# Optimization experiments

Measured on AMD Instinct MI355X. Metric: run time of the kernel, lower is better.

## Reference

```python
import jax, jax.numpy as jnp
import numpy as np

OUT_FEATURES = 4096
IN_FEATURES = 4096
GROUP_SIZE = 32
NUM_GROUPS = (OUT_FEATURES * IN_FEATURES) // GROUP_SIZE  # 524288, divisible by 8
PACKED_PER_GROUP = GROUP_SIZE * 3 // 8  # 12


def dequantize_3bit(x_packed, maxvals):
    # x_packed: [NUM_GROUPS * 12] int, values in [0,256) (uint8 bit patterns)
    # maxvals:  [NUM_GROUPS] float32 group scales
    G = NUM_GROUPS
    # view as [G, 4, 3]: 4 byte-triplets per group, each encoding 8 3-bit values
    p = x_packed.reshape(G, GROUP_SIZE // 8, 3)
    b0, b1, b2 = p[..., 0], p[..., 1], p[..., 2]
    v0 = b0 & 7
    v1 = (b0 >> 3) & 7
    v2 = ((b0 >> 6) & 3) | ((b1 & 1) << 2)
    v3 = (b1 >> 1) & 7
    v4 = (b1 >> 4) & 7
    v5 = ((b1 >> 7) & 1) | ((b2 & 3) << 1)
    v6 = (b2 >> 2) & 7
    v7 = (b2 >> 5) & 7
    q = jnp.stack([v0, v1, v2, v3, v4, v5, v6, v7], axis=-1)  # [G, 4, 8]
    q = q.reshape(G, GROUP_SIZE).astype(jnp.float32)
    x_norm = (q / 7.0 * 2.0 - 1.0) * maxvals[:, None]
    return x_norm.reshape(-1)  # [G * GROUP_SIZE]


def setup_inputs() -> dict:
    key = jax.random.key(0)
    k1, k2, k3, k4 = jax.random.split(key, 4)
    x = jax.random.normal(k1, (2, 2048, IN_FEATURES), dtype=jnp.float32)
    weight_q3 = jax.random.randint(k2, (NUM_GROUPS * PACKED_PER_GROUP,), 0, 256, dtype=jnp.int32)
    weight_norm = jax.random.uniform(k3, (NUM_GROUPS,), dtype=jnp.float32)
    bias = jax.random.normal(k4, (OUT_FEATURES,), dtype=jnp.float32)
    return {"x": x, "weight_q3": weight_q3, "weight_norm": weight_norm, "bias": bias}


def reference(x, weight_q3, weight_norm, bias):
    w_flat = dequantize_3bit(weight_q3, weight_norm)
    weight = w_flat[: OUT_FEATURES * IN_FEATURES].reshape(OUT_FEATURES, IN_FEATURES)
    # F.linear: y = x @ W.T + b
    return jnp.einsum("bsi,oi->bso", x, weight) + bias
```

## Files before the change

### kernel.cpp

```cpp
#include <hip/hip_runtime.h>

typedef unsigned short u16;
typedef unsigned int u32;

typedef __bf16 bf16x8 __attribute__((ext_vector_type(8)));
typedef float f32x4 __attribute__((ext_vector_type(4)));

#define OUT_F 4096
#define IN_F 4096
#define M_ROWS 4096
#define NUM_GROUPS ((OUT_F * IN_F) / 32)


__device__ __forceinline__ u16 f2bf(float f) {
    union { float f; u32 u; } c; c.f = f;
    u32 u = c.u;
    u += 0x7fffu + ((u >> 16) & 1u);
    return (u16)(u >> 16);
}

__device__ __forceinline__ u32 pk2(float a, float b) {
    return (u32)f2bf(a) | ((u32)f2bf(b) << 16);
}

__device__ __forceinline__ void async_copy16(const u16* g, u16* l) {
    __builtin_amdgcn_global_load_lds(
        (const __attribute__((address_space(1))) u32*)g,
        (__attribute__((address_space(3))) u32*)l,
        16, 0, 0);
}

__device__ __forceinline__ u32 lds_addr(const u16* p) {
    return (u32)(uintptr_t)(const __attribute__((address_space(3))) u16*)p;
}

__global__ __launch_bounds__(256) void prep_kernel(
        const float* __restrict__ x, const int* __restrict__ q,
        const float* __restrict__ scales,
        u16* __restrict__ W, u16* __restrict__ Xb) {
    int bid = blockIdx.x;
    int tid = threadIdx.x;
    if (bid < 8192) {
        int t = bid * 256 + tid;
        int b0 = q[3 * t];
        int b1 = q[3 * t + 1];
        int b2 = q[3 * t + 2];
        float mv = scales[t >> 2];
        float s = mv * (2.0f / 7.0f);
        float o = -mv;

        int v0 = b0 & 7;
        int v1 = (b0 >> 3) & 7;
        int v2 = ((b0 >> 6) & 3) | ((b1 & 1) << 2);
        int v3 = (b1 >> 1) & 7;
        int v4 = (b1 >> 4) & 7;
        int v5 = ((b1 >> 7) & 1) | ((b2 & 3) << 1);
        int v6 = (b2 >> 2) & 7;
        int v7 = (b2 >> 5) & 7;
        uint4 w;
        w.x = pk2(fmaf((float)v0, s, o), fmaf((float)v1, s, o));
        w.y = pk2(fmaf((float)v2, s, o), fmaf((float)v3, s, o));
        w.z = pk2(fmaf((float)v4, s, o), fmaf((float)v5, s, o));
        w.w = pk2(fmaf((float)v6, s, o), fmaf((float)v7, s, o));
        ((uint4*)W)[t] = w;
    } else {
        int i = (bid - 8192) * 256 + tid;
        const float4* p = (const float4*)x + (size_t)i * 2;
        float4 u = p[0], v = p[1];
        uint4 w;
        w.x = pk2(u.x, u.y);
        w.y = pk2(u.z, u.w);
        w.z = pk2(v.x, v.y);
        w.w = pk2(v.z, v.w);
        ((uint4*)Xb)[i] = w;
    }
}

__global__ __launch_bounds__(256, 2) void gemm_bt_kernel(
        const u16* __restrict__ A, const u16* __restrict__ B,
        const float* __restrict__ bias, float* __restrict__ C) {
    __shared__ u16 sA[256 * 64];
    __shared__ u16 sB[128 * 64];

    const int tid = threadIdx.x;
    const int lane = tid & 63;
    const int w = tid >> 6;
    const int wr = w >> 1;
    const int wc = w & 1;
    const int ln = lane & 15;
    const int quad = lane >> 4;
    const int lnx = ln & 7;

    const int lin = blockIdx.x;
    const int wg = (lin & 7) * 64 + (lin >> 3);
    const int mb = (wg >> 5) * 256;
    const int nb = (wg & 31) * 128;

    int offg[8], offl[8];
#pragma unroll
    for (int p = 0; p < 8; ++p) {
        int s = p * 256 + tid;
        int rl = s >> 3, pc = s & 7;
        int lc = pc ^ (rl & 7);
        offg[p] = rl * IN_F + lc * 8;
        offl[p] = s * 8;
    }
    const u16* baseA = A + (size_t)mb * IN_F;
    const u16* baseB = B + (size_t)nb * IN_F;

    const u32 sAb = lds_addr(sA);
    const u32 sBb = lds_addr(sB);
    const u32 aB0 = sAb + (u32)((wr * 128 + ln) * 128 + ((quad ^ lnx) * 16));
    const u32 aB1 = sAb + (u32)((wr * 128 + ln) * 128 + (((4 + quad) ^ lnx) * 16));
    const u32 bB0 = sBb + (u32)((wc * 64 + ln) * 128 + ((quad ^ lnx) * 16));
    const u32 bB1 = sBb + (u32)((wc * 64 + ln) * 128 + (((4 + quad) ^ lnx) * 16));

    float bj[4];
#pragma unroll
    for (int j = 0; j < 4; ++j)
        bj[j] = bias[nb + wc * 64 + j * 16 + ln];

    f32x4 acc[8][4];
#pragma unroll
    for (int i = 0; i < 8; ++i)
#pragma unroll
        for (int j = 0; j < 4; ++j) acc[i][j] = (f32x4)0.0f;

    bf16x8 av[4][2];
    bf16x8 bv[4][2];

#define DSR(dst, base, IMM) \
    asm volatile("ds_read_b128 %0, %1 offset:" #IMM \
                 : "=v"(dst) : "v"(base))

#define WAITG(N) \
    asm volatile("s_waitcnt lgkmcnt(" #N ")"); \
    __builtin_amdgcn_sched_barrier(0);

#define MROW(IR, ACR) \
    acc[ACR][0] = __builtin_amdgcn_mfma_f32_16x16x32_bf16( \
        av[IR][0], bv[0][0], acc[ACR][0], 0, 0, 0); \
    acc[ACR][1] = __builtin_amdgcn_mfma_f32_16x16x32_bf16( \
        av[IR][0], bv[1][0], acc[ACR][1], 0, 0, 0); \
    acc[ACR][2] = __builtin_amdgcn_mfma_f32_16x16x32_bf16( \
        av[IR][0], bv[2][0], acc[ACR][2], 0, 0, 0); \
    acc[ACR][3] = __builtin_amdgcn_mfma_f32_16x16x32_bf16( \
        av[IR][0], bv[3][0], acc[ACR][3], 0, 0, 0); \
    acc[ACR][0] = __builtin_amdgcn_mfma_f32_16x16x32_bf16( \
        av[IR][1], bv[0][1], acc[ACR][0], 0, 0, 0); \
    acc[ACR][1] = __builtin_amdgcn_mfma_f32_16x16x32_bf16( \
        av[IR][1], bv[1][1], acc[ACR][1], 0, 0, 0); \
    acc[ACR][2] = __builtin_amdgcn_mfma_f32_16x16x32_bf16( \
        av[IR][1], bv[2][1], acc[ACR][2], 0, 0, 0); \
    acc[ACR][3] = __builtin_amdgcn_mfma_f32_16x16x32_bf16( \
        av[IR][1], bv[3][1], acc[ACR][3], 0, 0, 0);

#pragma unroll
    for (int p = 0; p < 8; ++p)
        async_copy16(baseA + offg[p], &sA[offl[p]]);
#pragma unroll
    for (int p = 0; p < 4; ++p)
        async_copy16(baseB + offg[p], &sB[offl[p]]);
    asm volatile("s_waitcnt vmcnt(0)");
    __builtin_amdgcn_s_barrier();

#pragma unroll 1
    for (int t = 0; t < 64; ++t) {
        DSR(bv[0][0], bB0, 0);     DSR(bv[0][1], bB1, 0);
        DSR(bv[1][0], bB0, 2048);  DSR(bv[1][1], bB1, 2048);
        DSR(bv[2][0], bB0, 4096);  DSR(bv[2][1], bB1, 4096);
        DSR(bv[3][0], bB0, 6144);  DSR(bv[3][1], bB1, 6144);
        DSR(av[0][0], aB0, 0);     DSR(av[0][1], aB1, 0);
        DSR(av[1][0], aB0, 2048);  DSR(av[1][1], aB1, 2048);
        DSR(av[2][0], aB0, 4096);  DSR(av[2][1], aB1, 4096);
        DSR(av[3][0], aB0, 6144);  DSR(av[3][1], aB1, 6144);
        __builtin_amdgcn_s_setprio(1);
        WAITG(6); MROW(0, 0);
        WAITG(4); MROW(1, 1);
        WAITG(2); MROW(2, 2);
        WAITG(0); MROW(3, 3);
        __builtin_amdgcn_s_setprio(0);

        DSR(av[0][0], aB0, 8192);   DSR(av[0][1], aB1, 8192);
        DSR(av[1][0], aB0, 10240);  DSR(av[1][1], aB1, 10240);
        DSR(av[2][0], aB0, 12288);  DSR(av[2][1], aB1, 12288);
        DSR(av[3][0], aB0, 14336);  DSR(av[3][1], aB1, 14336);
        __builtin_amdgcn_s_setprio(1);
        WAITG(6); MROW(0, 4);
        WAITG(4); MROW(1, 5);
        WAITG(2); MROW(2, 6);
        WAITG(0); MROW(3, 7);
        __builtin_amdgcn_s_setprio(0);

        __builtin_amdgcn_s_barrier();
        if (t < 63) {
            const int ko1 = (t + 1) << 6;
#pragma unroll
            for (int p = 0; p < 8; ++p)
                async_copy16(baseA + offg[p] + ko1, &sA[offl[p]]);
#pragma unroll
            for (int p = 0; p < 4; ++p)
                async_copy16(baseB + offg[p] + ko1, &sB[offl[p]]);
        }
        asm volatile("s_waitcnt vmcnt(0)");
        __builtin_amdgcn_s_barrier();
    }

#undef DSR
#undef WAITG
#undef MROW

#pragma unroll
    for (int i = 0; i < 8; ++i) {
        const int mrow = mb + wr * 128 + i * 16 + quad * 4;
#pragma unroll
        for (int j = 0; j < 4; ++j) {
            const int col = nb + wc * 64 + j * 16 + ln;
            float* cp = C + (size_t)mrow * OUT_F + col;
#pragma unroll
            for (int r = 0; r < 4; ++r)
                cp[(size_t)r * OUT_F] = acc[i][j][r] + bj[j];
        }
    }
}

extern "C" void kernel_launch(void* const* d_in, const int* in_sizes, int n_in,
                              void* d_out, int out_size, void* d_ws, size_t ws_size,
                              hipStream_t stream) {
    const float* x = (const float*)d_in[0];
    const int* wq = (const int*)d_in[1];
    const float* wn = (const float*)d_in[2];
    const float* bias = (const float*)d_in[3];
    float* out = (float*)d_out;

    u16* Wb = (u16*)d_ws;
    u16* Xb = Wb + (size_t)OUT_F * IN_F;

    prep_kernel<<<16384, 256, 0, stream>>>(x, wq, wn, Wb, Xb);
    gemm_bt_kernel<<<512, 256, 0, stream>>>(Xb, Wb, bias, out);
}
```

Baseline: 141.0 us.

## Load B operand directly from global to registers and double-buffer A tile in LDS

The weight (B) operand is no longer staged through shared memory. Each lane now issues global_load_dwordx4 straight into its MFMA operand registers, and the next K-step's B loads are issued before the barrier. The A tile becomes double-buffered in LDS so the next tile's async copy overlaps the current compute, dropping one barrier and the full vmcnt(0) drain per iteration. This cuts LDS traffic and synchronisation, but adds uncoalesced-ish strided global reads for B, hand-managed vmcnt counting, and one redundant wrap-around prefetch on the final iteration.

Result: slower. 195.5 us (+38.6%).

```diff
diff --git a/kernel.cpp b/kernel.cpp
--- a/kernel.cpp
+++ b/kernel.cpp
@@ -2,6 +2,7 @@
 
 typedef unsigned short u16;
 typedef unsigned int u32;
+typedef unsigned long long u64;
 
 typedef __bf16 bf16x8 __attribute__((ext_vector_type(8)));
 typedef float f32x4 __attribute__((ext_vector_type(4)));
@@ -10,6 +11,8 @@
 #define IN_F 4096
 #define M_ROWS 4096
 #define NUM_GROUPS ((OUT_F * IN_F) / 32)
+
+#define TILE_A_E (256 * 64)
 
 
 __device__ __forceinline__ u16 f2bf(float f) {
@@ -79,8 +82,7 @@
 __global__ __launch_bounds__(256, 2) void gemm_bt_kernel(
         const u16* __restrict__ A, const u16* __restrict__ B,
         const float* __restrict__ bias, float* __restrict__ C) {
-    __shared__ u16 sA[256 * 64];
-    __shared__ u16 sB[128 * 64];
+    __shared__ u16 sA[2 * TILE_A_E];
 
     const int tid = threadIdx.x;
     const int lane = tid & 63;
@@ -106,14 +108,16 @@
         offl[p] = s * 8;
     }
     const u16* baseA = A + (size_t)mb * IN_F;
-    const u16* baseB = B + (size_t)nb * IN_F;
 
     const u32 sAb = lds_addr(sA);
-    const u32 sBb = lds_addr(sB);
     const u32 aB0 = sAb + (u32)((wr * 128 + ln) * 128 + ((quad ^ lnx) * 16));
     const u32 aB1 = sAb + (u32)((wr * 128 + ln) * 128 + (((4 + quad) ^ lnx) * 16));
-    const u32 bB0 = sBb + (u32)((wc * 64 + ln) * 128 + ((quad ^ lnx) * 16));
-    const u32 bB1 = sBb + (u32)((wc * 64 + ln) * 128 + (((4 + quad) ^ lnx) * 16));
+
+    u64 bAddr[4];
+#pragma unroll
+    for (int j = 0; j < 4; ++j)
+        bAddr[j] = (u64)(const char*)(B + (size_t)(nb + wc * 64 + j * 16 + ln) * IN_F)
+                 + (u64)(quad * 16);
 
     float bj[4];
 #pragma unroll
@@ -133,9 +137,38 @@
     asm volatile("ds_read_b128 %0, %1 offset:" #IMM \
                  : "=v"(dst) : "v"(base))
 
-#define WAITG(N) \
-    asm volatile("s_waitcnt lgkmcnt(" #N ")"); \
-    __builtin_amdgcn_sched_barrier(0);
+#define GLB0(dst, ap) \
+    asm volatile("global_load_dwordx4 %0, %1, off" : "=v"(dst) : "v"(ap))
+#define GLB1(dst, ap) \
+    asm volatile("global_load_dwordx4 %0, %1, off offset:64" : "=v"(dst) : "v"(ap))
+
+#define WVL(V, L) \
+    asm volatile("s_waitcnt vmcnt(" #V ") lgkmcnt(" #L ")"); \
+    __builtin_amdgcn_sched_barrier(0);
+#define WV(V) \
+    asm volatile("s_waitcnt vmcnt(" #V ")"); \
+    __builtin_amdgcn_sched_barrier(0);
+#define WL(L) \
+    asm volatile("s_waitcnt lgkmcnt(" #L ")"); \
+    __builtin_amdgcn_sched_barrier(0);
+
+#define MCOL(J) \
+    acc[0][J] = __builtin_amdgcn_mfma_f32_16x16x32_bf16( \
+        av[0][0], bv[J][0], acc[0][J], 0, 0, 0); \
+    acc[1][J] = __builtin_amdgcn_mfma_f32_16x16x32_bf16( \
+        av[1][0], bv[J][0], acc[1][J], 0, 0, 0); \
+    acc[2][J] = __builtin_amdgcn_mfma_f32_16x16x32_bf16( \
+        av[2][0], bv[J][0], acc[2][J], 0, 0, 0); \
+    acc[3][J] = __builtin_amdgcn_mfma_f32_16x16x32_bf16( \
+        av[3][0], bv[J][0], acc[3][J], 0, 0, 0); \
+    acc[0][J] = __builtin_amdgcn_mfma_f32_16x16x32_bf16( \
+        av[0][1], bv[J][1], acc[0][J], 0, 0, 0); \
+    acc[1][J] = __builtin_amdgcn_mfma_f32_16x16x32_bf16( \
+        av[1][1], bv[J][1], acc[1][J], 0, 0, 0); \
+    acc[2][J] = __builtin_amdgcn_mfma_f32_16x16x32_bf16( \
+        av[2][1], bv[J][1], acc[2][J], 0, 0, 0); \
+    acc[3][J] = __builtin_amdgcn_mfma_f32_16x16x32_bf16( \
+        av[3][1], bv[J][1], acc[3][J], 0, 0, 0);
 
 #define MROW(IR, ACR) \
     acc[ACR][0] = __builtin_amdgcn_mfma_f32_16x16x32_bf16( \
@@ -155,60 +188,78 @@
     acc[ACR][3] = __builtin_amdgcn_mfma_f32_16x16x32_bf16( \
         av[IR][1], bv[3][1], acc[ACR][3], 0, 0, 0);
 
+#define ISSUE_B() \
+    GLB0(bv[0][0], bAddr[0]); GLB1(bv[0][1], bAddr[0]); \
+    GLB0(bv[1][0], bAddr[1]); GLB1(bv[1][1], bAddr[1]); \
+    GLB0(bv[2][0], bAddr[2]); GLB1(bv[2][1], bAddr[2]); \
+    GLB0(bv[3][0], bAddr[3]); GLB1(bv[3][1], bAddr[3]);
+
 #pragma unroll
     for (int p = 0; p < 8; ++p)
         async_copy16(baseA + offg[p], &sA[offl[p]]);
-#pragma unroll
-    for (int p = 0; p < 4; ++p)
-        async_copy16(baseB + offg[p], &sB[offl[p]]);
     asm volatile("s_waitcnt vmcnt(0)");
     __builtin_amdgcn_s_barrier();
+    ISSUE_B();
+    __builtin_amdgcn_sched_barrier(0);
 
 #pragma unroll 1
     for (int t = 0; t < 64; ++t) {
-        DSR(bv[0][0], bB0, 0);     DSR(bv[0][1], bB1, 0);
-        DSR(bv[1][0], bB0, 2048);  DSR(bv[1][1], bB1, 2048);
-        DSR(bv[2][0], bB0, 4096);  DSR(bv[2][1], bB1, 4096);
-        DSR(bv[3][0], bB0, 6144);  DSR(bv[3][1], bB1, 6144);
-        DSR(av[0][0], aB0, 0);     DSR(av[0][1], aB1, 0);
-        DSR(av[1][0], aB0, 2048);  DSR(av[1][1], aB1, 2048);
-        DSR(av[2][0], aB0, 4096);  DSR(av[2][1], aB1, 4096);
-        DSR(av[3][0], aB0, 6144);  DSR(av[3][1], aB1, 6144);
+        const int cur = t & 1;
+        const u32 curOff = (u32)cur << 15;
+        const u32 aC0 = aB0 + curOff, aC1 = aB1 + curOff;
+        u16* aNx = sA + (cur ^ 1) * TILE_A_E;
+        const int ko1 = ((t + 1) & 63) << 6;
+
+#pragma unroll
+        for (int p = 0; p < 8; ++p)
+            async_copy16(baseA + offg[p] + ko1, &aNx[offl[p]]);
+        __builtin_amdgcn_sched_barrier(0);
+
+        DSR(av[0][0], aC0, 0);     DSR(av[0][1], aC1, 0);
+        DSR(av[1][0], aC0, 2048);  DSR(av[1][1], aC1, 2048);
+        DSR(av[2][0], aC0, 4096);  DSR(av[2][1], aC1, 4096);
+        DSR(av[3][0], aC0, 6144);  DSR(av[3][1], aC1, 6144);
         __builtin_amdgcn_s_setprio(1);
-        WAITG(6); MROW(0, 0);
-        WAITG(4); MROW(1, 1);
-        WAITG(2); MROW(2, 2);
-        WAITG(0); MROW(3, 3);
+        WVL(14, 0); MCOL(0);
+        WV(12);     MCOL(1);
+        WV(10);     MCOL(2);
+        WV(8);      MCOL(3);
+        __builtin_amdgcn_sched_barrier(0);
         __builtin_amdgcn_s_setprio(0);
 
-        DSR(av[0][0], aB0, 8192);   DSR(av[0][1], aB1, 8192);
-        DSR(av[1][0], aB0, 10240);  DSR(av[1][1], aB1, 10240);
-        DSR(av[2][0], aB0, 12288);  DSR(av[2][1], aB1, 12288);
-        DSR(av[3][0], aB0, 14336);  DSR(av[3][1], aB1, 14336);
+        DSR(av[0][0], aC0, 8192);   DSR(av[0][1], aC1, 8192);
+        DSR(av[1][0], aC0, 10240);  DSR(av[1][1], aC1, 10240);
+        DSR(av[2][0], aC0, 12288);  DSR(av[2][1], aC1, 12288);
+        DSR(av[3][0], aC0, 14336);  DSR(av[3][1], aC1, 14336);
         __builtin_amdgcn_s_setprio(1);
-        WAITG(6); MROW(0, 4);
-        WAITG(4); MROW(1, 5);
-        WAITG(2); MROW(2, 6);
-        WAITG(0); MROW(3, 7);
+        WL(6); MROW(0, 4);
+        WL(4); MROW(1, 5);
+        WL(2); MROW(2, 6);
+        WL(0); MROW(3, 7);
+        __builtin_amdgcn_sched_barrier(0);
         __builtin_amdgcn_s_setprio(0);
 
+#pragma unroll
+        for (int j = 0; j < 4; ++j) bAddr[j] += 128;
+        ISSUE_B();
+        __builtin_amdgcn_sched_barrier(0);
+
+        WV(8);
         __builtin_amdgcn_s_barrier();
-        if (t < 63) {
-            const int ko1 = (t + 1) << 6;
-#pragma unroll
-            for (int p = 0; p < 8; ++p)
-                async_copy16(baseA + offg[p] + ko1, &sA[offl[p]]);
-#pragma unroll
-            for (int p = 0; p < 4; ++p)
-                async_copy16(baseB + offg[p] + ko1, &sB[offl[p]]);
-        }
-        asm volatile("s_waitcnt vmcnt(0)");
-        __builtin_amdgcn_s_barrier();
     }
 
 #undef DSR
-#undef WAITG
+#undef GLB0
+#undef GLB1
+#undef WVL
+#undef WV
+#undef WL
+#undef MCOL
 #undef MROW
+#undef ISSUE_B
+
+    asm volatile("s_waitcnt vmcnt(0) lgkmcnt(0)");
+    __builtin_amdgcn_sched_barrier(0);
 
 #pragma unroll
     for (int i = 0; i < 8; ++i) {
```
